# Optimization experiments

Measured on AMD Instinct MI355X. Metric: run time of the kernel, lower is better.

The kernel has to match this reference:

```python
import jax, jax.numpy as jnp
import numpy as np

B, C, H, W = 32, 256, 64, 64
S, K = 128, 8  # NUM_CHANNEL_SETS, MAX_CHANNELS_PER_SET


def setup_inputs() -> dict:
    key = jax.random.key(0)
    kx, ki = jax.random.split(key)
    x = jax.random.normal(kx, (B, C, H, W), dtype=jnp.float32)
    channel_idx_sets = jax.random.randint(ki, (S, K), 0, C, dtype=jnp.int32)
    return {"x": x, "channel_idx_sets": channel_idx_sets}


def reference(x, channel_idx_sets):
    # Gather channels for each set, then max-reduce over the set dimension.
    # x: [B, C, H, W]; channel_idx_sets: [S, K] int32 -> out: [B, S, H, W]
    gathered = x[:, channel_idx_sets, :, :]  # [B, S, K, H, W]
    return jnp.max(gathered, axis=2)
```

## Files before the change

### kernel.cpp

```cpp
#include <hip/hip_runtime.h>


constexpr int Bb = 32, Cc = 256, Hh = 64, Ww = 64, Ss = 128, Kk = 8;
constexpr int HW4 = (Hh * Ww) / 4;

typedef float f4 __attribute__((ext_vector_type(4)));

__global__ __launch_bounds__(256) void fmp_kernel(
    const f4* __restrict__ x4,
    const int* __restrict__ idx,
    f4*       __restrict__ out4)
{
    const unsigned bid   = blockIdx.x;
    const unsigned xcd   = bid & 7u;
    const unsigned t     = bid >> 3;
    const unsigned phase = t >> 9;
    const unsigned rest  = t & 511u;
    const unsigned b     = xcd + 8u * phase;
    const unsigned s     = rest >> 2;
    const unsigned chunk = rest & 3u;
    const unsigned hw4   = chunk * 256u + threadIdx.x;

    const int* __restrict__ ip = idx + s * Kk;
    const f4* __restrict__ xb = x4 + (size_t)b * (Cc * HW4) + hw4;

    f4 m = xb[(size_t)ip[0] * HW4];
    #pragma unroll
    for (int k = 1; k < Kk; ++k) {
        const f4 v = xb[(size_t)ip[k] * HW4];
        m.x = fmaxf(m.x, v.x);
        m.y = fmaxf(m.y, v.y);
        m.z = fmaxf(m.z, v.z);
        m.w = fmaxf(m.w, v.w);
    }

    const size_t o = (((size_t)b * Ss + s) * HW4) + hw4;
    __builtin_nontemporal_store(m, &out4[o]);
}

extern "C" void kernel_launch(void* const* d_in, const int* in_sizes, int n_in,
                              void* d_out, int out_size, void* d_ws, size_t ws_size,
                              hipStream_t stream) {
    const f4*  x4  = (const f4*)d_in[0];
    const int* idx = (const int*)d_in[1];
    f4*        o4  = (f4*)d_out;

    const int n4     = Bb * Ss * Hh * Ww / 4;
    const int blocks = n4 / 256;
    fmp_kernel<<<blocks, 256, 0, stream>>>(x4, idx, o4);
}
```

Before: 218.4 us.

## Stage all channels of a spatial chunk in LDS and gather from shared memory

Each block now loads one 32-float spatial chunk for all 256 channels of one batch into LDS, using async global-to-LDS loads. It then computes all 128 channel-set maxima from LDS. Previously each output re-gathered 8 channels from global memory, so the input was read many times over. Now each input element is read from global memory once. The cost is 32KB of LDS per block, a barrier, possible LDS bank conflicts on the random-index reads, and reliance on the 16-byte global_load_lds builtin.

```diff
diff --git a/kernel.cpp b/kernel.cpp
--- a/kernel.cpp
+++ b/kernel.cpp
@@ -2,40 +2,69 @@
 
 
 constexpr int Bb = 32, Cc = 256, Hh = 64, Ww = 64, Ss = 128, Kk = 8;
-constexpr int HW4 = (Hh * Ww) / 4;
+constexpr int CHUNKF4 = 8;
+constexpr int NCHUNK  = (Hh * Ww / 4) / CHUNKF4;
+constexpr int PLANEF4 = Hh * Ww / 4;
 
 typedef float f4 __attribute__((ext_vector_type(4)));
+typedef int   i4 __attribute__((ext_vector_type(4)));
+
+__device__ __forceinline__ f4 fmax4(f4 a, f4 b) {
+    f4 r;
+    r.x = fmaxf(a.x, b.x);
+    r.y = fmaxf(a.y, b.y);
+    r.z = fmaxf(a.z, b.z);
+    r.w = fmaxf(a.w, b.w);
+    return r;
+}
 
 __global__ __launch_bounds__(256) void fmp_kernel(
     const f4* __restrict__ x4,
     const int* __restrict__ idx,
     f4*       __restrict__ out4)
 {
-    const unsigned bid   = blockIdx.x;
-    const unsigned xcd   = bid & 7u;
-    const unsigned t     = bid >> 3;
-    const unsigned phase = t >> 9;
-    const unsigned rest  = t & 511u;
-    const unsigned b     = xcd + 8u * phase;
-    const unsigned s     = rest >> 2;
-    const unsigned chunk = rest & 3u;
-    const unsigned hw4   = chunk * 256u + threadIdx.x;
+    __shared__ f4 lds[Cc * CHUNKF4];
 
-    const int* __restrict__ ip = idx + s * Kk;
-    const f4* __restrict__ xb = x4 + (size_t)b * (Cc * HW4) + hw4;
+    const int t     = threadIdx.x;
+    const int b     = blockIdx.x >> 7;
+    const int chunk = blockIdx.x & (NCHUNK - 1);
+    const int j     = t & 7;
+    const int c0    = t >> 3;
 
-    f4 m = xb[(size_t)ip[0] * HW4];
+    const f4* gbase = x4 + (size_t)b * (Cc * PLANEF4) + chunk * CHUNKF4 + j;
     #pragma unroll
-    for (int k = 1; k < Kk; ++k) {
-        const f4 v = xb[(size_t)ip[k] * HW4];
-        m.x = fmaxf(m.x, v.x);
-        m.y = fmaxf(m.y, v.y);
-        m.z = fmaxf(m.z, v.z);
-        m.w = fmaxf(m.w, v.w);
+    for (int r = 0; r < 8; ++r) {
+        const f4* g = gbase + (size_t)(c0 + 32 * r) * PLANEF4;
+        __builtin_amdgcn_global_load_lds(
+            (const __attribute__((address_space(1))) void*)g,
+            (__attribute__((address_space(3))) void*)&lds[t + 256 * r],
+            16, 0, 0);
     }
 
-    const size_t o = (((size_t)b * Ss + s) * HW4) + hw4;
-    __builtin_nontemporal_store(m, &out4[o]);
+    i4 ia[4], ib[4];
+    #pragma unroll
+    for (int r = 0; r < 4; ++r) {
+        const i4* ir = (const i4*)(idx + (c0 + 32 * r) * Kk);
+        ia[r] = ir[0];
+        ib[r] = ir[1];
+    }
+
+    __syncthreads();
+
+    const size_t obase = (size_t)b * (Ss * PLANEF4) + chunk * CHUNKF4 + j;
+    #pragma unroll
+    for (int r = 0; r < 4; ++r) {
+        const int s = c0 + 32 * r;
+        f4 m =        lds[ia[r].x * CHUNKF4 + j];
+        m = fmax4(m,  lds[ia[r].y * CHUNKF4 + j]);
+        m = fmax4(m,  lds[ia[r].z * CHUNKF4 + j]);
+        m = fmax4(m,  lds[ia[r].w * CHUNKF4 + j]);
+        m = fmax4(m,  lds[ib[r].x * CHUNKF4 + j]);
+        m = fmax4(m,  lds[ib[r].y * CHUNKF4 + j]);
+        m = fmax4(m,  lds[ib[r].z * CHUNKF4 + j]);
+        m = fmax4(m,  lds[ib[r].w * CHUNKF4 + j]);
+        __builtin_nontemporal_store(m, &out4[obase + (size_t)s * PLANEF4]);
+    }
 }
 
 extern "C" void kernel_launch(void* const* d_in, const int* in_sizes, int n_in,
@@ -45,7 +74,6 @@
     const int* idx = (const int*)d_in[1];
     f4*        o4  = (f4*)d_out;
 
-    const int n4     = Bb * Ss * Hh * Ww / 4;
-    const int blocks = n4 / 256;
+    const int blocks = Bb * NCHUNK;
     fmp_kernel<<<blocks, 256, 0, stream>>>(x4, idx, o4);
 }
```

New measurement: 214.3 us. About the same (-1.9%).
